# Performance work log

Measured on AMD Instinct MI355X. Metric: run time of the kernel, lower is better.

Reference implementation:

```python
import jax, jax.numpy as jnp
import numpy as np

BATCH = 32768
NUM_CLASSES = 1024  # balanced binary hierarchy => 10 levels, 1023 internal nodes


def setup_inputs() -> dict:
    key = jax.random.key(0)
    outputs = jax.random.normal(key, (BATCH, NUM_CLASSES), dtype=jnp.float32)
    return {"outputs": outputs}


def reference(outputs) -> jnp.ndarray:
    """SoftEmbeddedDecisionRules.forward for a balanced binary hierarchy.

    For every internal node: child logit = mean of raw logits over the child's
    leaf (class) set, softmax over the node's children, then multiply each
    class's running probability by the prob of the branch containing it.
    With a balanced binary tree over C classes, level l has 2^l nodes, each
    child covering a contiguous block of C / 2^(l+1) classes, so the per-node
    Python loop of the original collapses into one reshape+mean+softmax per
    level (log2(C) fused passes total).
    """
    B, C = outputs.shape
    depth = C.bit_length() - 1  # log2(C), static
    class_probs = jnp.ones((B, C), dtype=outputs.dtype)
    for level in range(depth):
        n_nodes = 1 << level
        seg = C // (2 * n_nodes)  # classes per child subtree
        # node logits: mean of raw logits over each child's class block
        node_logits = outputs.reshape(B, n_nodes, 2, seg).mean(axis=-1)  # [B, n, 2]
        probs = jax.nn.softmax(node_logits, axis=-1)  # softmax over children
        # scatter-multiply child prob onto every class in that child's subtree
        expanded = jnp.broadcast_to(probs[..., None], (B, n_nodes, 2, seg)).reshape(B, C)
        class_probs = class_probs * expanded
    return class_probs
```

## Files before the change

### kernel.cpp

```cpp
#include <hip/hip_runtime.h>


#define C 1024

__global__ __launch_bounds__(256) void hier_softmax_kernel(
    const float* __restrict__ in, float* __restrict__ out) {
    __shared__ float heap[512];
    __shared__ float pleft[256];

    const int row = blockIdx.x;
    const int tid = threadIdx.x;

    const float4 v = ((const float4*)(in + (size_t)row * C))[tid];

    const float s2a = v.x + v.y;
    const float s2b = v.z + v.w;
    const float s4  = s2a + s2b;
    heap[256 + tid] = s4;
    __syncthreads();

    for (int cnt = 128; cnt >= 1; cnt >>= 1) {
        if (tid < cnt) {
            const int n = cnt + tid;
            const float a = heap[2 * n];
            const float b = heap[2 * n + 1];
            heap[n] = a + b;
            const float inv_seg = (float)cnt * (1.0f / 512.0f);
            pleft[n] = 1.0f / (1.0f + __expf((b - a) * inv_seg));
        }
        __syncthreads();
    }

    float common = 1.0f;
    const int leaf = 256 + tid;
#pragma unroll
    for (int s = 7; s >= 0; --s) {
        const int m = leaf >> s;
        const float p = pleft[m >> 1];
        common *= (m & 1) ? (1.0f - p) : p;
    }

    const float p9 = 1.0f / (1.0f + __expf((s2b - s2a) * 0.5f));
    const float pA = 1.0f / (1.0f + __expf(v.y - v.x));
    const float pB = 1.0f / (1.0f + __expf(v.w - v.z));

    const float cl = common * p9;
    const float cr = common * (1.0f - p9);
    float4 o;
    o.x = cl * pA;
    o.y = cl * (1.0f - pA);
    o.z = cr * pB;
    o.w = cr * (1.0f - pB);
    ((float4*)(out + (size_t)row * C))[tid] = o;
}

extern "C" void kernel_launch(void* const* d_in, const int* in_sizes, int n_in,
                              void* d_out, int out_size, void* d_ws, size_t ws_size,
                              hipStream_t stream) {
    const float* in = (const float*)d_in[0];
    float* out = (float*)d_out;
    const int B = in_sizes[0] / C;
    hier_softmax_kernel<<<B, 256, 0, stream>>>(in, out);
}
```

Before: 218.2 us.

## Replace shared-memory heap tree with wave shuffle butterfly for node probabilities

Replaces the eight-step shared-memory reduction tree, with its barrier after every level, by an xor-shuffle butterfly inside each 64-lane wave. Each lane computes the sigmoid for its own side at every level, followed by one cross-wave exchange through a four-entry shared array and a single barrier. This removes most barriers and shared-memory traffic, and it uses a hardware reciprocal for the sigmoid. In exchange, every lane now evaluates redundant exponentials, and the reduction order changes slightly, which can shift rounding.

```diff
diff --git a/kernel.cpp b/kernel.cpp
--- a/kernel.cpp
+++ b/kernel.cpp
@@ -3,54 +3,55 @@
 
 #define C 1024
 
+__device__ __forceinline__ float sigmoid_of(float x) {
+    return __builtin_amdgcn_rcpf(1.0f + __expf(x));
+}
+
 __global__ __launch_bounds__(256) void hier_softmax_kernel(
     const float* __restrict__ in, float* __restrict__ out) {
-    __shared__ float heap[512];
-    __shared__ float pleft[256];
+    __shared__ float wsum[4];
 
     const int row = blockIdx.x;
     const int tid = threadIdx.x;
+    const int wave = tid >> 6;
+    const int lane = tid & 63;
 
     const float4 v = ((const float4*)(in + (size_t)row * C))[tid];
 
     const float s2a = v.x + v.y;
     const float s2b = v.z + v.w;
-    const float s4  = s2a + s2b;
-    heap[256 + tid] = s4;
+    float sum = s2a + s2b;
+
+    const float pA = sigmoid_of(v.y - v.x);
+    const float pB = sigmoid_of(v.w - v.z);
+    const float p9 = sigmoid_of((s2b - s2a) * 0.5f);
+
+    float common = 1.0f;
+    float inv_seg = 0.25f;
+#pragma unroll
+    for (int k = 1; k <= 32; k <<= 1) {
+        const float partner = __shfl_xor(sum, k, 64);
+        common *= sigmoid_of((partner - sum) * inv_seg);
+        sum += partner;
+        inv_seg *= 0.5f;
+    }
+
+    if (lane == 0) wsum[wave] = sum;
     __syncthreads();
 
-    for (int cnt = 128; cnt >= 1; cnt >>= 1) {
-        if (tid < cnt) {
-            const int n = cnt + tid;
-            const float a = heap[2 * n];
-            const float b = heap[2 * n + 1];
-            heap[n] = a + b;
-            const float inv_seg = (float)cnt * (1.0f / 512.0f);
-            pleft[n] = 1.0f / (1.0f + __expf((b - a) * inv_seg));
-        }
-        __syncthreads();
-    }
-
-    float common = 1.0f;
-    const int leaf = 256 + tid;
-#pragma unroll
-    for (int s = 7; s >= 0; --s) {
-        const int m = leaf >> s;
-        const float p = pleft[m >> 1];
-        common *= (m & 1) ? (1.0f - p) : p;
-    }
-
-    const float p9 = 1.0f / (1.0f + __expf((s2b - s2a) * 0.5f));
-    const float pA = 1.0f / (1.0f + __expf(v.y - v.x));
-    const float pB = 1.0f / (1.0f + __expf(v.w - v.z));
+    const float partnerW = wsum[wave ^ 1];
+    common *= sigmoid_of((partnerW - sum) * (1.0f / 256.0f));
+    const float myHalf = sum + partnerW;
+    const float otherHalf = wsum[wave ^ 2] + wsum[wave ^ 3];
+    common *= sigmoid_of((otherHalf - myHalf) * (1.0f / 512.0f));
 
     const float cl = common * p9;
-    const float cr = common * (1.0f - p9);
+    const float cr = common - cl;
     float4 o;
     o.x = cl * pA;
-    o.y = cl * (1.0f - pA);
+    o.y = cl - o.x;
     o.z = cr * pB;
-    o.w = cr * (1.0f - pB);
+    o.w = cr - o.z;
     ((float4*)(out + (size_t)row * C))[tid] = o;
 }
 
```

After: 216.5 us. Within noise of the previous version (-0.8%).
